# Performance work log

Measured on AMD Instinct MI355X. Metric: run time of the kernel, lower is better.

## Reference

```python
import jax, jax.numpy as jnp
import numpy as np

D = 256      # dim_model
H = 8        # n_head
FFN = 1024
L = 2        # n_layers
WIN = 100.0  # window_size of LocalisedEncoding
MINWL = 0.01 # min_wavelength of LocalisedEncoding
EPS = 1e-5


def _mass_sinusoid(mz):
    # depthcharge MassEncoder: min_wavelength=0.001, max_wavelength=10000
    n_sin = D // 2
    n_cos = D - n_sin
    base = 0.001 / (2.0 * np.pi)
    scale = 10000.0 / 0.001
    sin_term = (base * scale ** (np.arange(n_sin) / (n_sin - 1))).astype(np.float32)
    cos_term = (base * scale ** (np.arange(n_cos) / (n_cos - 1))).astype(np.float32)
    return jnp.concatenate([jnp.sin(mz / sin_term), jnp.cos(mz / cos_term)], axis=-1)


def _pe_lookup(pe, mass):
    # LocalisedEncoding.forward: clamp, linear index into precomputed table
    m = jnp.clip(mass, -WIN, WIN)
    idx = ((m + 1.0 + WIN) / MINWL).astype(jnp.int32)
    return pe[idx]


def _ln(x, g, b):
    mu = jnp.mean(x, axis=-1, keepdims=True)
    var = jnp.mean((x - mu) ** 2, axis=-1, keepdims=True)
    return (x - mu) * jax.lax.rsqrt(var + EPS) * g + b


def _forward(spectra, pe, latent, int_w, in_w, in_b, out_w, out_b,
             l1_w, l1_b, l2_w, l2_b, n1_g, n1_b, n2_g, n2_b):
    B, Np, _ = spectra.shape
    pad = jnp.sum(spectra, axis=2) == 0  # padded peaks
    # CustomPeakEncoder with mass=None, precursor_mass=None, dim_intensity=None
    peaks = _mass_sinusoid(spectra[:, :, :1]) + spectra[:, :, 1:2] @ int_w.T
    x = jnp.concatenate([jnp.broadcast_to(latent, (B, 1, D)), peaks], axis=1)
    mask = jnp.concatenate([jnp.zeros((B, 1), bool), pad], axis=1)  # [B,N]
    masses = jnp.concatenate([jnp.zeros((B, 1), spectra.dtype), spectra[:, :, 0]], axis=1)
    N = Np + 1
    hd = D // H
    scale = 1.0 / np.sqrt(hd)
    neg = jnp.asarray(-1e9, x.dtype)

    for l in range(L):
        wq, wk, wv = in_w[l, :D], in_w[l, D:2 * D], in_w[l, 2 * D:]
        bq, bk, bv = in_b[l, :D], in_b[l, D:2 * D], in_b[l, 2 * D:]
        if l == 0:
            # localized path: relative mass-difference encoding added to K/V
            pe0 = _pe_lookup(pe, jnp.zeros((), x.dtype))          # [D]
            q_in = x + pe0                                         # [B,N,D]
            rel = masses[:, None, :] - masses[:, :, None]          # m_j - m_i, [B,N,N]
            kv_in = x[:, None, :, :] + _pe_lookup(pe, rel)         # [B,N,N,D]
            Q = (q_in @ wq.T + bq).reshape(B, N, H, hd)
            K = (kv_in @ wk.T + bk).reshape(B, N, N, H, hd)
            V = (kv_in @ wv.T + bv).reshape(B, N, N, H, hd)
            s = jnp.einsum('bihd,bijhd->bhij', Q, K) * scale
            s = jnp.where(mask[:, None, None, :], neg, s)
            a = jax.nn.softmax(s, axis=-1)
            y = jnp.einsum('bhij,bijhd->bihd', a, V).reshape(B, N, D)
        else:
            Q = (x @ wq.T + bq).reshape(B, N, H, hd)
            K = (x @ wk.T + bk).reshape(B, N, H, hd)
            V = (x @ wv.T + bv).reshape(B, N, H, hd)
            s = jnp.einsum('bihd,bjhd->bhij', Q, K) * scale
            s = jnp.where(mask[:, None, None, :], neg, s)
            a = jax.nn.softmax(s, axis=-1)
            y = jnp.einsum('bhij,bjhd->bihd', a, V).reshape(B, N, D)
        y = y @ out_w[l].T + out_b[l]
        x = _ln(x + y, n1_g[l], n1_b[l])
        f = jax.nn.relu(x @ l1_w[l].T + l1_b[l]) @ l2_w[l].T + l2_b[l]
        x = _ln(x + f, n2_g[l], n2_b[l])
    return x


def setup_inputs() -> dict:
    key = jax.random.key(0)
    ks = jax.random.split(key, 14)
    B, Np = 16, 150
    mz = jax.random.uniform(ks[0], (B, Np, 1), dtype=jnp.float32) * 300.0
    inten = jax.random.uniform(ks[1], (B, Np, 1), dtype=jnp.float32)
    spectra = jnp.concatenate([mz, inten], axis=-1)
    # zero-pad the last 20 peaks of every other spectrum
    pad = (jnp.arange(Np)[None, :] >= 130) & (jnp.arange(B)[:, None] % 2 == 0)
    spectra = jnp.where(pad[:, :, None], 0.0, spectra)

    # LocalisedEncoding precomputed pe buffer (casanovo_style=True)
    max_len = int((WIN + 1) * 2 / MINWL)  # 20200
    pos = np.arange(max_len) - max_len // 2
    div = np.exp(np.arange(0, D, 2) * (-np.log(10000.0) / D))
    pe_np = np.zeros((max_len, D), np.float32)
    pe_np[:, : D // 2] = np.sin(pos[:, None] * div)
    pe_np[:, D // 2:] = np.cos(pos[:, None] * div)

    s = 0.05
    return {
        'spectra': spectra,
        'pe': jnp.asarray(pe_np),
        'latent': jax.random.normal(ks[2], (1, 1, D), jnp.float32) * s,
        'int_w': jax.random.normal(ks[3], (D, 1), jnp.float32) * s,
        'in_w': jax.random.normal(ks[4], (L, 3 * D, D), jnp.float32) * s,
        'in_b': jax.random.normal(ks[5], (L, 3 * D), jnp.float32) * s,
        'out_w': jax.random.normal(ks[6], (L, D, D), jnp.float32) * s,
        'out_b': jax.random.normal(ks[7], (L, D), jnp.float32) * s,
        'l1_w': jax.random.normal(ks[8], (L, FFN, D), jnp.float32) * s,
        'l1_b': jax.random.normal(ks[9], (L, FFN), jnp.float32) * s,
        'l2_w': jax.random.normal(ks[10], (L, D, FFN), jnp.float32) * s,
        'l2_b': jax.random.normal(ks[11], (L, D), jnp.float32) * s,
        'n1_g': jnp.ones((L, D), jnp.float32),
        'n1_b': jnp.zeros((L, D), jnp.float32),
        'n2_g': jnp.ones((L, D), jnp.float32),
        'n2_b': jnp.zeros((L, D), jnp.float32),
    }


def reference(spectra, pe, latent, int_w, in_w, in_b, out_w, out_b,
              l1_w, l1_b, l2_w, l2_b, n1_g, n1_b, n2_g, n2_b):
    return _forward(spectra, pe, latent, int_w, in_w, in_b, out_w, out_b,
                    l1_w, l1_b, l2_w, l2_b, n1_g, n1_b, n2_g, n2_b)
```

## Files before the change

kernel.cpp:

```cpp
#include <hip/hip_runtime.h>
#include <hip/hip_bf16.h>
#include <math.h>

#define BB 16
#define NP 150
#define NN 151
#define DD 256
#define HH 8
#define HD 32
#define FFN_ 1024
#define PE_LEN 20200
#define ROWS (BB*NN)
#define MPAD 2432
#define PE_PAD 20224


typedef __attribute__((ext_vector_type(8))) short short8;
typedef __attribute__((ext_vector_type(4))) float f32x4;
typedef __attribute__((ext_vector_type(4))) unsigned u32x4;

#if defined(__has_builtin)
#if __has_builtin(__builtin_amdgcn_fdot2_f32_bf16)
#define HAVE_DOT2 1
#endif
#endif
#ifndef HAVE_DOT2
#define HAVE_DOT2 0
#endif

__device__ __forceinline__ float r16(float x) {
    return __bfloat162float(__float2bfloat16(x));
}
__device__ __forceinline__ float us2f(unsigned short u) {
    return __uint_as_float((unsigned)u << 16);
}
__device__ __forceinline__ float lo2f(unsigned x) {
    return __uint_as_float(x << 16);
}
__device__ __forceinline__ float hi2f(unsigned x) {
    return __uint_as_float(x & 0xFFFF0000u);
}
__device__ __forceinline__ unsigned cvtpk(float lo, float hi) {
    unsigned r;
    asm("v_cvt_pk_bf16_f32 %0, %1, %2" : "=v"(r) : "v"(lo), "v"(hi));
    return r;
}
#if HAVE_DOT2
typedef __attribute__((ext_vector_type(2))) __bf16 bf16x2;
__device__ __forceinline__ float dot2bf(unsigned a, unsigned b, float acc) {
    bf16x2 av = __builtin_bit_cast(bf16x2, a);
    bf16x2 bv = __builtin_bit_cast(bf16x2, b);
    return __builtin_amdgcn_fdot2_f32_bf16(av, bv, acc, false);
}
#endif

#define PACK_BLOCKS 1024
__global__ __launch_bounds__(256) void buildpack_kernel(
    const float* __restrict__ spectra, const float* __restrict__ latent,
    const float* __restrict__ int_w, const float* __restrict__ pe,
    float* __restrict__ x, __hip_bfloat16* __restrict__ xb,
    __hip_bfloat16* __restrict__ xqb,
    float* __restrict__ masses, float* __restrict__ maskf,
    const float* __restrict__ in_w,  __hip_bfloat16* __restrict__ inw_p,
    const float* __restrict__ out_w, __hip_bfloat16* __restrict__ outw_p,
    const float* __restrict__ l1_w,  __hip_bfloat16* __restrict__ l1w_p,
    const float* __restrict__ l2_w,  __hip_bfloat16* __restrict__ l2w_p,
    __hip_bfloat16* __restrict__ pe_p)
{
    int tid = threadIdx.x;
    if (blockIdx.x < ROWS) {
        int bn = blockIdx.x;
        int b = bn / NN, n = bn % NN;
        float val;
        if (n == 0) {
            val = latent[tid];
            if (tid == 0) { masses[bn] = 0.0f; maskf[bn] = 0.0f; }
        } else {
            float mz = spectra[(b*NP + n - 1)*2 + 0];
            float it = spectra[(b*NP + n - 1)*2 + 1];
            int i = (tid < 128) ? tid : tid - 128;
            const double base_d = 0.001 / (2.0 * 3.141592653589793);
            double term_d = base_d * pow(1.0e7, (double)i / 127.0);
            float tf = (float)term_d;
            double arg = (double)mz / (double)tf;
            double sv = (tid < 128) ? sin(arg) : cos(arg);
            val = (float)sv + it * int_w[tid];
            if (tid == 0) {
                masses[bn] = mz;
                maskf[bn] = ((mz + it) == 0.0f) ? 1.0f : 0.0f;
            }
        }
        x[bn*DD + tid] = val;
        xb[bn*DD + tid] = __float2bfloat16(val);
        xqb[bn*DD + tid] = __float2bfloat16(val + pe[10100*DD + tid]);
    } else {
        long long base = (long long)(blockIdx.x - ROWS) * 256 + tid;
        const long long stride = (long long)PACK_BLOCKS * 256;
        for (long long i = base; i < (long long)PE_PAD*DD; i += stride)
            pe_p[i] = __float2bfloat16(i < (long long)PE_LEN*DD ? pe[i] : 0.0f);
        for (long long i = base; i < 2LL*768*DD; i += stride)
            inw_p[i] = __float2bfloat16(in_w[i]);
        for (long long i = base; i < 2LL*DD*DD; i += stride)
            outw_p[i] = __float2bfloat16(out_w[i]);
        for (long long i = base; i < 2LL*FFN_*DD; i += stride)
            l1w_p[i] = __float2bfloat16(l1_w[i]);
        for (long long i = base; i < 2LL*DD*FFN_; i += stride)
            l2w_p[i] = __float2bfloat16(l2_w[i]);
    }
}

template<typename CT>
__global__ __launch_bounds__(256) void gemm_mfma(
    const __hip_bfloat16* __restrict__ A, const __hip_bfloat16* __restrict__ W,
    const float* __restrict__ bias, CT* __restrict__ C,
    int M, int Nc, int K, int ldc, int relu)
{
    int wave = threadIdx.x >> 6;
    int lane = threadIdx.x & 63;
    int NT = Nc >> 5;
    int MT = (M + 31) >> 5;
    int id = blockIdx.x * 4 + wave;
    if (id >= MT * NT) return;
    int mt = id / NT, nt = id % NT;
    int m0 = mt * 32, n0 = nt * 32;
    int rl = lane & 15, q8 = (lane >> 4) * 8;

    const short8* Ap0 = (const short8*)(A + (size_t)(m0 + rl)*K + q8);
    const short8* Ap1 = (const short8*)(A + (size_t)(m0 + 16 + rl)*K + q8);
    const short8* Wp0 = (const short8*)(W + (size_t)(n0 + rl)*K + q8);
    const short8* Wp1 = (const short8*)(W + (size_t)(n0 + 16 + rl)*K + q8);

    f32x4 acc00 = {0,0,0,0}, acc01 = {0,0,0,0};
    f32x4 acc10 = {0,0,0,0}, acc11 = {0,0,0,0};
    int steps = K >> 5;
    for (int s = 0; s < steps; ++s) {
        short8 a0 = Ap0[s*4];
        short8 a1 = Ap1[s*4];
        short8 b0 = Wp0[s*4];
        short8 b1 = Wp1[s*4];
        acc00 = __builtin_amdgcn_mfma_f32_16x16x32_bf16(a0, b0, acc00, 0, 0, 0);
        acc01 = __builtin_amdgcn_mfma_f32_16x16x32_bf16(a0, b1, acc01, 0, 0, 0);
        acc10 = __builtin_amdgcn_mfma_f32_16x16x32_bf16(a1, b0, acc10, 0, 0, 0);
        acc11 = __builtin_amdgcn_mfma_f32_16x16x32_bf16(a1, b1, acc11, 0, 0, 0);
    }

    int rbase = (lane >> 4) * 4;
    #pragma unroll
    for (int sm = 0; sm < 2; ++sm) {
        #pragma unroll
        for (int sn = 0; sn < 2; ++sn) {
            f32x4 a = (sm == 0) ? (sn == 0 ? acc00 : acc01)
                                : (sn == 0 ? acc10 : acc11);
            int gc = n0 + sn*16 + rl;
            float bv = bias ? r16(bias[gc]) : 0.0f;
            #pragma unroll
            for (int rg = 0; rg < 4; ++rg) {
                int gr = m0 + sm*16 + rbase + rg;
                if (gr < M) {
                    float val = r16(a[rg]);
                    if (bias) val = r16(val + bv);
                    if (relu) val = fmaxf(val, 0.0f);
                    C[(size_t)gr*ldc + gc] = (CT)val;
                }
            }
        }
    }
}

template<int K>
__global__ __launch_bounds__(256) void gemm_skinny(
    const __hip_bfloat16* __restrict__ A, const __hip_bfloat16* __restrict__ W,
    const float* __restrict__ bias, float* __restrict__ C,
    int M, int Nc, int ldc)
{
    int NT = Nc >> 5;
    int id = blockIdx.x;
    int mt = id / NT, nt = id % NT;
    int m0 = mt * 16, n0 = nt * 32;
    int wave = threadIdx.x >> 6;
    int lane = threadIdx.x & 63;
    int rl = lane & 15, q8 = (lane >> 4) * 8;
    const int K4 = K >> 2;
    int k0 = wave * K4;

    const short8* Ap  = (const short8*)(A + (size_t)(m0 + rl)*K + k0 + q8);
    const short8* Wp0 = (const short8*)(W + (size_t)(n0 + rl)*K + k0 + q8);
    const short8* Wp1 = (const short8*)(W + (size_t)(n0 + 16 + rl)*K + k0 + q8);

    f32x4 acc0 = {0,0,0,0}, acc1 = {0,0,0,0};
    #pragma unroll
    for (int s = 0; s < K4/32; ++s) {
        short8 a  = Ap[s*4];
        short8 b0 = Wp0[s*4];
        short8 b1 = Wp1[s*4];
        acc0 = __builtin_amdgcn_mfma_f32_16x16x32_bf16(a, b0, acc0, 0, 0, 0);
        acc1 = __builtin_amdgcn_mfma_f32_16x16x32_bf16(a, b1, acc1, 0, 0, 0);
    }

    __shared__ float red[4][8][65];
    #pragma unroll
    for (int rg = 0; rg < 4; ++rg) {
        red[wave][rg][lane]   = acc0[rg];
        red[wave][4+rg][lane] = acc1[rg];
    }
    __syncthreads();

    #pragma unroll
    for (int t = 0; t < 2; ++t) {
        int sl = wave*2 + t;
        float s = red[0][sl][lane] + red[1][sl][lane]
                + red[2][sl][lane] + red[3][sl][lane];
        int rg = sl & 3, sn = sl >> 2;
        int gr = m0 + (lane >> 4)*4 + rg;
        int gc = n0 + sn*16 + rl;
        float val = r16(s);
        val = r16(val + r16(bias[gc]));
        if (gr < M) C[(size_t)gr*ldc + gc] = val;
    }
}

#define PEKV_BLK 632u
#define QKV0_BLK 456u

__device__ __forceinline__ void pekv_body(
    unsigned bid, int wave, int lane,
    const __hip_bfloat16* __restrict__ A, const __hip_bfloat16* __restrict__ W,
    __hip_bfloat16* __restrict__ C)
{
    const int K = 256, Nc = 512, ldc = 512, M = PE_LEN;
    int NT = Nc >> 5;
    int MT4 = (M + 127) >> 7;
    int id = bid * 4 + wave;
    if (id >= MT4 * NT) return;
    int mt = id / NT, nt = id % NT;
    int m0 = mt * 128, n0 = nt * 32;
    int rl = lane & 15, q8 = (lane >> 4) * 8;

    const short8* Ab  = (const short8*)(A + (size_t)(m0 + rl)*K + q8);
    const short8* Wp0 = (const short8*)(W + (size_t)(n0 + rl)*K + q8);
    const short8* Wp1 = (const short8*)(W + (size_t)(n0 + 16 + rl)*K + q8);
    const int rstep = K >> 3;

    f32x4 acc[4][2][2] = {};
    for (int s = 0; s < 8; ++s) {
        short8 b0 = Wp0[s*4];
        short8 b1 = Wp1[s*4];
        short8 a[4][2];
        #pragma unroll
        for (int t = 0; t < 4; ++t) {
            a[t][0] = Ab[(size_t)(t*32)*rstep + s*4];
            a[t][1] = Ab[(size_t)(t*32+16)*rstep + s*4];
        }
        #pragma unroll
        for (int t = 0; t < 4; ++t) {
            acc[t][0][0] = __builtin_amdgcn_mfma_f32_16x16x32_bf16(a[t][0], b0, acc[t][0][0], 0, 0, 0);
            acc[t][0][1] = __builtin_amdgcn_mfma_f32_16x16x32_bf16(a[t][0], b1, acc[t][0][1], 0, 0, 0);
            acc[t][1][0] = __builtin_amdgcn_mfma_f32_16x16x32_bf16(a[t][1], b0, acc[t][1][0], 0, 0, 0);
            acc[t][1][1] = __builtin_amdgcn_mfma_f32_16x16x32_bf16(a[t][1], b1, acc[t][1][1], 0, 0, 0);
        }
    }

    int rbase = (lane >> 4) * 4;
    #pragma unroll
    for (int t = 0; t < 4; ++t) {
        #pragma unroll
        for (int sm = 0; sm < 2; ++sm) {
            #pragma unroll
            for (int sn = 0; sn < 2; ++sn) {
                f32x4 a = acc[t][sm][sn];
                int gc = n0 + sn*16 + rl;
                #pragma unroll
                for (int rg = 0; rg < 4; ++rg) {
                    int gr = m0 + t*32 + sm*16 + rbase + rg;
                    if (gr < M)
                        C[(size_t)gr*ldc + gc] = (__hip_bfloat16)r16(a[rg]);
                }
            }
        }
    }
}

__device__ __forceinline__ void qkv0_body(
    unsigned bid, int wave, int lane,
    const __hip_bfloat16* __restrict__ xqb, const __hip_bfloat16* __restrict__ xb,
    const __hip_bfloat16* __restrict__ inw_p, const float* __restrict__ in_b,
    __hip_bfloat16* __restrict__ qb, __hip_bfloat16* __restrict__ kvb, int M)
{
    int MT = (M + 31) >> 5;
    int id = bid * 4 + wave;
    if (id >= MT * 24) return;
    int mt = id / 24, ntt = id % 24;
    bool isQ = (ntt < 8);
    const __hip_bfloat16* A = isQ ? xqb : xb;
    const __hip_bfloat16* W = inw_p + (isQ ? (size_t)ntt*32*DD
                                           : (size_t)(256 + (ntt-8)*32)*DD);
    const float* bias = in_b + (isQ ? ntt*32 : 256 + (ntt-8)*32);
    __hip_bfloat16* C = isQ ? qb : kvb;
    int ldc = isQ ? 256 : 512;
    int cbase = isQ ? ntt*32 : (ntt-8)*32;
    int m0 = mt * 32;
    int rl = lane & 15, q8 = (lane >> 4) * 8;
    const int K = DD;

    const short8* Ap0 = (const short8*)(A + (size_t)(m0 + rl)*K + q8);
    const short8* Ap1 = (const short8*)(A + (size_t)(m0 + 16 + rl)*K + q8);
    const short8* Wp0 = (const short8*)(W + (size_t)(rl)*K + q8);
    const short8* Wp1 = (const short8*)(W + (size_t)(16 + rl)*K + q8);

    f32x4 acc00 = {0,0,0,0}, acc01 = {0,0,0,0};
    f32x4 acc10 = {0,0,0,0}, acc11 = {0,0,0,0};
    for (int s = 0; s < K/32; ++s) {
        short8 a0 = Ap0[s*4];
        short8 a1 = Ap1[s*4];
        short8 b0 = Wp0[s*4];
        short8 b1 = Wp1[s*4];
        acc00 = __builtin_amdgcn_mfma_f32_16x16x32_bf16(a0, b0, acc00, 0, 0, 0);
        acc01 = __builtin_amdgcn_mfma_f32_16x16x32_bf16(a0, b1, acc01, 0, 0, 0);
        acc10 = __builtin_amdgcn_mfma_f32_16x16x32_bf16(a1, b0, acc10, 0, 0, 0);
        acc11 = __builtin_amdgcn_mfma_f32_16x16x32_bf16(a1, b1, acc11, 0, 0, 0);
    }

    int rbase = (lane >> 4) * 4;
    #pragma unroll
    for (int sm = 0; sm < 2; ++sm) {
        #pragma unroll
        for (int sn = 0; sn < 2; ++sn) {
            f32x4 a = (sm == 0) ? (sn == 0 ? acc00 : acc01)
                                : (sn == 0 ? acc10 : acc11);
            int gc = cbase + sn*16 + rl;
            float bv = r16(bias[sn*16 + rl]);
            #pragma unroll
            for (int rg = 0; rg < 4; ++rg) {
                int gr = m0 + sm*16 + rbase + rg;
                if (gr < M) {
                    float val = r16(a[rg]);
                    val = r16(val + bv);
                    C[(size_t)gr*ldc + gc] = (__hip_bfloat16)val;
                }
            }
        }
    }
}

__global__ __launch_bounds__(256) void pekv_qkv0_kernel(
    const __hip_bfloat16* __restrict__ pe_p, const __hip_bfloat16* __restrict__ wkv0,
    __hip_bfloat16* __restrict__ pekv,
    const __hip_bfloat16* __restrict__ xqb, const __hip_bfloat16* __restrict__ xb,
    const __hip_bfloat16* __restrict__ inw_p, const float* __restrict__ in_b,
    __hip_bfloat16* __restrict__ qb, __hip_bfloat16* __restrict__ kvb)
{
    int wave = threadIdx.x >> 6;
    int lane = threadIdx.x & 63;
    if (blockIdx.x < PEKV_BLK)
        pekv_body(blockIdx.x, wave, lane, pe_p, wkv0, pekv);
    else
        qkv0_body(blockIdx.x - PEKV_BLK, wave, lane, xqb, xb, inw_p, in_b,
                  qb, kvb, ROWS);
}

template<bool USE_PE, int QS, int KS, int VS>
__global__ __launch_bounds__(256) void attn_kernel(
    const __hip_bfloat16* __restrict__ qp,
    const __hip_bfloat16* __restrict__ kp,
    const __hip_bfloat16* __restrict__ vp,
    const __hip_bfloat16* __restrict__ pekv,
    const float* __restrict__ masses, const float* __restrict__ maskf,
    __hip_bfloat16* __restrict__ yb)
{
    int b = blockIdx.x & 15;
    int i = blockIdx.x >> 4;
    int tid = threadIdx.x;
    int c = tid & 31;
    int g = tid >> 5;
    int h = c >> 2;

    __shared__ float sc[HH][152];
    __shared__ float msh[152];
    __shared__ int   tj[152];
    __shared__ __align__(16) float part[8][264];

    if (tid < NN) {
        msh[tid] = maskf[b*NN + tid];
        if (USE_PE) {
            double m = (double)masses[b*NN + tid] - (double)masses[b*NN + i];
            m = fmin(fmax(m, -100.0), 100.0);
            tj[tid] = (int)(((m + 1.0) + 100.0) / 0.01);
        }
    }

    unsigned qw[4];
    {
        const u32x4 q4 = *(const u32x4*)((const unsigned short*)qp
                            + (size_t)(b*NN + i)*QS + c*8);
        qw[0] = q4[0]; qw[1] = q4[1]; qw[2] = q4[2]; qw[3] = q4[3];
    }
#if !HAVE_DOT2
    float qf[8];
    #pragma unroll
    for (int w = 0; w < 4; ++w) { qf[2*w] = lo2f(qw[w]); qf[2*w+1] = hi2f(qw[w]); }
#endif
    __syncthreads();

    const float scale = 0.17677669529663687f;
    const unsigned short* kbase = (const unsigned short*)kp + (size_t)(b*NN)*KS + c*8;
    const unsigned short* vbase = (const unsigned short*)vp + (size_t)(b*NN)*VS + c*8;
    const unsigned short* pkb = (const unsigned short*)pekv + c*8;
    const unsigned short* pvb = (const unsigned short*)pekv + 256 + c*8;

    {
        int j = g;
        u32x4 kcur = *(const u32x4*)(kbase + (size_t)j*KS);
        u32x4 pcur;
        if (USE_PE) pcur = *(const u32x4*)(pkb + (size_t)tj[j]*512);
        for (int p = 0; p < 19; ++p) {
            int jn = j + 8;
            bool more = (jn < NN);
            u32x4 kn, pn;
            if (more) {
                kn = *(const u32x4*)(kbase + (size_t)jn*KS);
                if (USE_PE) pn = *(const u32x4*)(pkb + (size_t)tj[jn]*512);
            }
            float acc = 0.0f;
#if HAVE_DOT2
            #pragma unroll
            for (int w = 0; w < 4; ++w) {
                unsigned kd = kcur[w];
                if (USE_PE) {
                    unsigned pd = pcur[w];
                    float s0 = lo2f(kd) + lo2f(pd);
                    float s1 = hi2f(kd) + hi2f(pd);
                    kd = cvtpk(s0, s1);
                }
                acc = dot2bf(qw[w], kd, acc);
            }
#else
            #pragma unroll
            for (int w = 0; w < 4; ++w) {
                unsigned kd = kcur[w];
                float k0 = lo2f(kd), k1 = hi2f(kd);
                if (USE_PE) {
                    unsigned pd = pcur[w];
                    k0 = r16(k0 + lo2f(pd));
                    k1 = r16(k1 + hi2f(pd));
                }
                acc = fmaf(qf[2*w], k0, acc);
                acc = fmaf(qf[2*w+1], k1, acc);
            }
#endif
            acc += __shfl_xor(acc, 1);
            acc += __shfl_xor(acc, 2);
            if ((c & 3) == 0) {
                float s = acc * scale;
                if (msh[j] != 0.0f) s = -1e9f;
                sc[h][j] = s;
            }
            if (!more) break;
            j = jn; kcur = kn;
            if (USE_PE) pcur = pn;
        }
    }
    __syncthreads();

    {
        int lane = tid & 31;
        int hh = g;
        float mx = -INFINITY;
        for (int j = lane; j < NN; j += 32) mx = fmaxf(mx, sc[hh][j]);
        #pragma unroll
        for (int off = 16; off; off >>= 1) mx = fmaxf(mx, __shfl_xor(mx, off, 32));
        float sum = 0.0f;
        for (int j = lane; j < NN; j += 32) {
            float e = expf(sc[hh][j] - mx);
            sc[hh][j] = e;
            sum += e;
        }
        #pragma unroll
        for (int off = 16; off; off >>= 1) sum += __shfl_xor(sum, off, 32);
        float inv = 1.0f / sum;
        for (int j = lane; j < NN; j += 32) sc[hh][j] = r16(sc[hh][j] * inv);
    }
    __syncthreads();

    {
        float ya[8];
        #pragma unroll
        for (int u = 0; u < 8; ++u) ya[u] = 0.0f;

#if HAVE_DOT2
        u32x4 vA = *(const u32x4*)(vbase + (size_t)g*VS);
        u32x4 vB = *(const u32x4*)(vbase + (size_t)(g+8)*VS);
        u32x4 pA, pB;
        if (USE_PE) {
            pA = *(const u32x4*)(pvb + (size_t)tj[g]*512);
            pB = *(const u32x4*)(pvb + (size_t)tj[g+8]*512);
        }
        for (int t = 0; t < 9; ++t) {
            int jA = g + t*16, jB = jA + 8;
            u32x4 nvA, nvB, npA, npB;
            if (t < 8) {
                int nA = jA + 16, nB = jB + 16;
                nvA = *(const u32x4*)(vbase + (size_t)nA*VS);
                nvB = *(const u32x4*)(vbase + (size_t)nB*VS);
                if (USE_PE) {
                    npA = *(const u32x4*)(pvb + (size_t)tj[nA]*512);
                    npB = *(const u32x4*)(pvb + (size_t)tj[nB]*512);
                }
            }
            unsigned apair = cvtpk(sc[h][jA], sc[h][jB]);
            #pragma unroll
            for (int w = 0; w < 4; ++w) {
                unsigned lopair, hipair;
                if (USE_PE) {
                    float sA0 = lo2f(vA[w]) + lo2f(pA[w]);
                    float sA1 = hi2f(vA[w]) + hi2f(pA[w]);
                    float sB0 = lo2f(vB[w]) + lo2f(pB[w]);
                    float sB1 = hi2f(vB[w]) + hi2f(pB[w]);
                    lopair = cvtpk(sA0, sB0);
                    hipair = cvtpk(sA1, sB1);
                } else {
                    lopair = __builtin_amdgcn_perm(vB[w], vA[w], 0x05040100u);
                    hipair = __builtin_amdgcn_perm(vB[w], vA[w], 0x07060302u);
                }
                ya[2*w]   = dot2bf(apair, lopair, ya[2*w]);
                ya[2*w+1] = dot2bf(apair, hipair, ya[2*w+1]);
            }
            if (t < 8) {
                vA = nvA; vB = nvB;
                if (USE_PE) { pA = npA; pB = npB; }
            }
        }
        if (g + 144 < NN) {
            int jT = g + 144;
            u32x4 v = *(const u32x4*)(vbase + (size_t)jT*VS);
            u32x4 pq;
            if (USE_PE) pq = *(const u32x4*)(pvb + (size_t)tj[jT]*512);
            float aT = sc[h][jT];
            #pragma unroll
            for (int w = 0; w < 4; ++w) {
                float v0 = lo2f(v[w]), v1 = hi2f(v[w]);
                if (USE_PE) {
                    unsigned pk2 = cvtpk(v0 + lo2f(pq[w]), v1 + hi2f(pq[w]));
                    v0 = lo2f(pk2); v1 = hi2f(pk2);
                }
                ya[2*w]   = fmaf(aT, v0, ya[2*w]);
                ya[2*w+1] = fmaf(aT, v1, ya[2*w+1]);
            }
        }
#else
        int j = g;
        u32x4 vcur = *(const u32x4*)(vbase + (size_t)j*VS);
        u32x4 pcur;
        if (USE_PE) pcur = *(const u32x4*)(pvb + (size_t)tj[j]*512);
        float acur = sc[h][j];
        for (int p = 0; p < 19; ++p) {
            int jn = j + 8;
            bool more = (jn < NN);
            u32x4 vn, pn;
            float an = 0.0f;
            if (more) {
                vn = *(const u32x4*)(vbase + (size_t)jn*VS);
                if (USE_PE) pn = *(const u32x4*)(pvb + (size_t)tj[jn]*512);
                an = sc[h][jn];
            }
            #pragma unroll
            for (int w = 0; w < 4; ++w) {
                float v0 = lo2f(vcur[w]), v1 = hi2f(vcur[w]);
                if (USE_PE) {
                    v0 = r16(v0 + lo2f(pcur[w]));
                    v1 = r16(v1 + hi2f(pcur[w]));
                }
                ya[2*w]   = fmaf(acur, v0, ya[2*w]);
                ya[2*w+1] = fmaf(acur, v1, ya[2*w+1]);
            }
            if (!more) break;
            j = jn; vcur = vn; acur = an;
            if (USE_PE) pcur = pn;
        }
#endif
        f32x4* pp = (f32x4*)&part[g][c*8];
        pp[0] = f32x4{ya[0], ya[1], ya[2], ya[3]};
        pp[1] = f32x4{ya[4], ya[5], ya[6], ya[7]};
    }
    __syncthreads();

    {
        float s = part[0][tid];
        #pragma unroll
        for (int g2 = 1; g2 < 8; ++g2) s += part[g2][tid];
        yb[(size_t)(b*NN + i)*DD + tid] = __float2bfloat16(s);
    }
}

template<bool WRITE_B>
__global__ __launch_bounds__(256) void add_ln_kernel(
    const float* __restrict__ xin, const float* __restrict__ res,
    const float* __restrict__ g, const float* __restrict__ bb,
    float* __restrict__ xout, __hip_bfloat16* __restrict__ xbout)
{
    int r = blockIdx.x; int tid = threadIdx.x;
    float v = xin[r*DD + tid] + res[r*DD + tid];
    __shared__ float red[4];
    float s = v;
    #pragma unroll
    for (int off = 32; off; off >>= 1) s += __shfl_xor(s, off);
    if ((tid & 63) == 0) red[tid >> 6] = s;
    __syncthreads();
    float mu = (red[0] + red[1] + red[2] + red[3]) * (1.0f/256.0f);
    __syncthreads();
    float d = v - mu;
    float s2 = d*d;
    #pragma unroll
    for (int off = 32; off; off >>= 1) s2 += __shfl_xor(s2, off);
    if ((tid & 63) == 0) red[tid >> 6] = s2;
    __syncthreads();
    float var = (red[0] + red[1] + red[2] + red[3]) * (1.0f/256.0f);
    float out = d * (1.0f / sqrtf(var + 1e-5f)) * g[tid] + bb[tid];
    xout[r*DD + tid] = out;
    if (WRITE_B) xbout[r*DD + tid] = __float2bfloat16(out);
}

extern "C" void kernel_launch(void* const* d_in, const int* in_sizes, int n_in,
                              void* d_out, int out_size, void* d_ws, size_t ws_size,
                              hipStream_t stream)
{
    const float* spectra = (const float*)d_in[0];
    const float* pe      = (const float*)d_in[1];
    const float* latent  = (const float*)d_in[2];
    const float* int_w   = (const float*)d_in[3];
    const float* in_w    = (const float*)d_in[4];
    const float* in_b    = (const float*)d_in[5];
    const float* out_w   = (const float*)d_in[6];
    const float* out_b   = (const float*)d_in[7];
    const float* l1_w    = (const float*)d_in[8];
    const float* l1_b    = (const float*)d_in[9];
    const float* l2_w    = (const float*)d_in[10];
    const float* l2_b    = (const float*)d_in[11];
    const float* n1_g    = (const float*)d_in[12];
    const float* n1_b    = (const float*)d_in[13];
    const float* n2_g    = (const float*)d_in[14];
    const float* n2_b    = (const float*)d_in[15];

    float* x      = (float*)d_ws;
    float* y2     = x      + ROWS*DD;
    float* masses = y2     + ROWS*DD;
    float* maskf  = masses + ROWS;
    __hip_bfloat16* bp = (__hip_bfloat16*)(maskf + ROWS);
    __hip_bfloat16* xb    = bp;  bp += (size_t)MPAD*DD;
    __hip_bfloat16* xqb   = bp;  bp += (size_t)MPAD*DD;
    __hip_bfloat16* qb    = bp;  bp += (size_t)MPAD*DD;
    __hip_bfloat16* kvb   = bp;  bp += (size_t)MPAD*768;
    __hip_bfloat16* yb    = bp;  bp += (size_t)MPAD*DD;
    __hip_bfloat16* f1b   = bp;  bp += (size_t)MPAD*FFN_;
    __hip_bfloat16* pekv  = bp;  bp += (size_t)PE_PAD*512;
    __hip_bfloat16* pe_p  = bp;  bp += (size_t)PE_PAD*DD;
    __hip_bfloat16* inw_p = bp;  bp += (size_t)2*768*DD;
    __hip_bfloat16* outw_p= bp;  bp += (size_t)2*DD*DD;
    __hip_bfloat16* l1w_p = bp;  bp += (size_t)2*FFN_*DD;
    __hip_bfloat16* l2w_p = bp;  bp += (size_t)2*DD*FFN_;

    dim3 blk(256);
    auto GG = [](int M, int Nc){ return dim3((unsigned)((((M+31)>>5)*(Nc>>5) + 3) / 4)); };
    const unsigned SKINNY = (ROWS/16) * (256 >> 5);

    buildpack_kernel<<<ROWS + PACK_BLOCKS, blk, 0, stream>>>(
        spectra, latent, int_w, pe, x, xb, xqb, masses, maskf,
        in_w, inw_p, out_w, outw_p, l1_w, l1w_p, l2_w, l2w_p, pe_p);

    pekv_qkv0_kernel<<<PEKV_BLK + QKV0_BLK, blk, 0, stream>>>(
        pe_p, inw_p + 256*DD, pekv, xqb, xb, inw_p, in_b, qb, kvb);

    attn_kernel<true,256,512,512><<<ROWS, blk, 0, stream>>>(
        qb, kvb, kvb + 256, pekv, masses, maskf, yb);
    gemm_skinny<256><<<SKINNY, blk, 0, stream>>>(
        yb, outw_p, out_b, y2, ROWS, 256, 256);
    add_ln_kernel<true><<<ROWS, blk, 0, stream>>>(x, y2, n1_g, n1_b, x, xb);
    gemm_mfma<__hip_bfloat16><<<GG(ROWS, 1024), blk, 0, stream>>>(
        xb, l1w_p, l1_b, f1b, ROWS, 1024, 256, 1024, 1);
    gemm_skinny<1024><<<SKINNY, blk, 0, stream>>>(
        f1b, l2w_p, l2_b, y2, ROWS, 256, 256);
    add_ln_kernel<true><<<ROWS, blk, 0, stream>>>(x, y2, n2_g, n2_b, x, xb);

    gemm_mfma<__hip_bfloat16><<<GG(ROWS, 768), blk, 0, stream>>>(
        xb, inw_p + 768*DD, in_b + 768, kvb, ROWS, 768, 256, 768, 0);
    attn_kernel<false,768,768,768><<<ROWS, blk, 0, stream>>>(
        kvb, kvb + 256, kvb + 512, nullptr, masses, maskf, yb);
    gemm_skinny<256><<<SKINNY, blk, 0, stream>>>(
        yb, outw_p + 256*DD, out_b + 256, y2, ROWS, 256, 256);
    add_ln_kernel<true><<<ROWS, blk, 0, stream>>>(x, y2, n1_g + 256, n1_b + 256, x, xb);
    gemm_mfma<__hip_bfloat16><<<GG(ROWS, 1024), blk, 0, stream>>>(
        xb, l1w_p + FFN_*DD, l1_b + 1024, f1b, ROWS, 1024, 256, 1024, 1);
    gemm_skinny<1024><<<SKINNY, blk, 0, stream>>>(
        f1b, l2w_p + DD*FFN_, l2_b + 256, y2, ROWS, 256, 256);
    add_ln_kernel<false><<<ROWS, blk, 0, stream>>>(x, y2, n2_g + 256, n2_b + 256,
                                                   (float*)d_out, nullptr);
}
```

Measured before the change: 304.0 us.

## Precompute Q·K attention scores with MFMA GEMM before attention kernels

Adds a gemm_sqk kernel that computes the per-head Q·K^T score matrices with 16x16x32 bf16 MFMA into a padded fp32 workspace. The attention kernels then load these scores instead of doing scalar dot products against K. In layer 0 only the Q·PE_k term is still computed in-kernel and added to the loaded score. This replaces scalar score work with matrix instructions, but adds two kernel launches and an fp32 score buffer round trip through global memory. It also changes rounding, since (q·k + q·pe) is no longer the dot product of q with the bf16-rounded k+pe.

```diff
diff --git a/kernel.cpp b/kernel.cpp
--- a/kernel.cpp
+++ b/kernel.cpp
@@ -13,6 +13,7 @@
 #define ROWS (BB*NN)
 #define MPAD 2432
 #define PE_PAD 20224
+#define SQS 160
 
 
 typedef __attribute__((ext_vector_type(8))) short short8;
@@ -219,6 +220,35 @@
     }
 }
 
+template<int QS, int KS>
+__global__ __launch_bounds__(256) void gemm_sqk(
+    const __hip_bfloat16* __restrict__ Q, const __hip_bfloat16* __restrict__ Kp,
+    float* __restrict__ S)
+{
+    int wave = threadIdx.x >> 6;
+    int lane = threadIdx.x & 63;
+    int id = blockIdx.x * 4 + wave;
+    if (id >= 16*8*100) return;
+    int jt = id % 10, it = (id / 10) % 10;
+    int h = (id / 100) & 7, b = id / 800;
+    int i0 = it * 16, j0 = jt * 16;
+    int rl = lane & 15, q8 = (lane >> 4) * 8;
+
+    short8 a  = *(const short8*)(Q  + (size_t)(b*NN + i0 + rl)*QS + h*32 + q8);
+    short8 kb = *(const short8*)(Kp + (size_t)(b*NN + j0 + rl)*KS + h*32 + q8);
+    f32x4 acc = {0,0,0,0};
+    acc = __builtin_amdgcn_mfma_f32_16x16x32_bf16(a, kb, acc, 0, 0, 0);
+
+    float* Sb = S + ((size_t)(b*8 + h))*SQS*SQS;
+    int rbase = (lane >> 4) * 4;
+    #pragma unroll
+    for (int rg = 0; rg < 4; ++rg) {
+        int ii = i0 + rbase + rg, jj = j0 + rl;
+        if (ii < NN && jj < NN)
+            Sb[(size_t)ii*SQS + jj] = acc[rg];
+    }
+}
+
 #define PEKV_BLK 632u
 #define QKV0_BLK 456u
 
@@ -358,12 +388,12 @@
                   qb, kvb, ROWS);
 }
 
-template<bool USE_PE, int QS, int KS, int VS>
+template<bool USE_PE, int QS, int VS>
 __global__ __launch_bounds__(256) void attn_kernel(
     const __hip_bfloat16* __restrict__ qp,
-    const __hip_bfloat16* __restrict__ kp,
     const __hip_bfloat16* __restrict__ vp,
     const __hip_bfloat16* __restrict__ pekv,
+    const float* __restrict__ sqk,
     const float* __restrict__ masses, const float* __restrict__ maskf,
     __hip_bfloat16* __restrict__ yb)
 {
@@ -373,6 +403,7 @@
     int c = tid & 31;
     int g = tid >> 5;
     int h = c >> 2;
+    const float scale = 0.17677669529663687f;
 
     __shared__ float sc[HH][152];
     __shared__ float msh[152];
@@ -380,86 +411,77 @@
     __shared__ __align__(16) float part[8][264];
 
     if (tid < NN) {
-        msh[tid] = maskf[b*NN + tid];
+        float mval = maskf[b*NN + tid];
+        msh[tid] = mval;
         if (USE_PE) {
             double m = (double)masses[b*NN + tid] - (double)masses[b*NN + i];
             m = fmin(fmax(m, -100.0), 100.0);
             tj[tid] = (int)(((m + 1.0) + 100.0) / 0.01);
         }
+        const float* Sb = sqk + ((size_t)(b*8))*SQS*SQS + (size_t)i*SQS + tid;
+        if (USE_PE) {
+            #pragma unroll
+            for (int hh = 0; hh < 8; ++hh)
+                sc[hh][tid] = Sb[(size_t)hh*SQS*SQS];
+        } else {
+            #pragma unroll
+            for (int hh = 0; hh < 8; ++hh) {
+                float s = Sb[(size_t)hh*SQS*SQS] * scale;
+                sc[hh][tid] = (mval != 0.0f) ? -1e9f : s;
+            }
+        }
     }
 
     unsigned qw[4];
-    {
+#if !HAVE_DOT2
+    float qf[8];
+#endif
+    if (USE_PE) {
         const u32x4 q4 = *(const u32x4*)((const unsigned short*)qp
                             + (size_t)(b*NN + i)*QS + c*8);
         qw[0] = q4[0]; qw[1] = q4[1]; qw[2] = q4[2]; qw[3] = q4[3];
-    }
 #if !HAVE_DOT2
-    float qf[8];
-    #pragma unroll
-    for (int w = 0; w < 4; ++w) { qf[2*w] = lo2f(qw[w]); qf[2*w+1] = hi2f(qw[w]); }
+        #pragma unroll
+        for (int w = 0; w < 4; ++w) { qf[2*w] = lo2f(qw[w]); qf[2*w+1] = hi2f(qw[w]); }
 #endif
+    }
     __syncthreads();
 
-    const float scale = 0.17677669529663687f;
-    const unsigned short* kbase = (const unsigned short*)kp + (size_t)(b*NN)*KS + c*8;
     const unsigned short* vbase = (const unsigned short*)vp + (size_t)(b*NN)*VS + c*8;
     const unsigned short* pkb = (const unsigned short*)pekv + c*8;
     const unsigned short* pvb = (const unsigned short*)pekv + 256 + c*8;
 
-    {
+    if (USE_PE) {
         int j = g;
-        u32x4 kcur = *(const u32x4*)(kbase + (size_t)j*KS);
-        u32x4 pcur;
-        if (USE_PE) pcur = *(const u32x4*)(pkb + (size_t)tj[j]*512);
+        u32x4 pcur = *(const u32x4*)(pkb + (size_t)tj[j]*512);
         for (int p = 0; p < 19; ++p) {
             int jn = j + 8;
             bool more = (jn < NN);
-            u32x4 kn, pn;
-            if (more) {
-                kn = *(const u32x4*)(kbase + (size_t)jn*KS);
-                if (USE_PE) pn = *(const u32x4*)(pkb + (size_t)tj[jn]*512);
-            }
+            u32x4 pn;
+            if (more) pn = *(const u32x4*)(pkb + (size_t)tj[jn]*512);
             float acc = 0.0f;
 #if HAVE_DOT2
             #pragma unroll
+            for (int w = 0; w < 4; ++w) acc = dot2bf(qw[w], pcur[w], acc);
+#else
+            #pragma unroll
             for (int w = 0; w < 4; ++w) {
-                unsigned kd = kcur[w];
-                if (USE_PE) {
-                    unsigned pd = pcur[w];
-                    float s0 = lo2f(kd) + lo2f(pd);
-                    float s1 = hi2f(kd) + hi2f(pd);
-                    kd = cvtpk(s0, s1);
-                }
-                acc = dot2bf(qw[w], kd, acc);
-            }
-#else
-            #pragma unroll
-            for (int w = 0; w < 4; ++w) {
-                unsigned kd = kcur[w];
-                float k0 = lo2f(kd), k1 = hi2f(kd);
-                if (USE_PE) {
-                    unsigned pd = pcur[w];
-                    k0 = r16(k0 + lo2f(pd));
-                    k1 = r16(k1 + hi2f(pd));
-                }
-                acc = fmaf(qf[2*w], k0, acc);
-                acc = fmaf(qf[2*w+1], k1, acc);
+                acc = fmaf(qf[2*w],   lo2f(pcur[w]), acc);
+                acc = fmaf(qf[2*w+1], hi2f(pcur[w]), acc);
             }
 #endif
             acc += __shfl_xor(acc, 1);
             acc += __shfl_xor(acc, 2);
             if ((c & 3) == 0) {
-                float s = acc * scale;
+                float s = (sc[h][j] + acc) * scale;
                 if (msh[j] != 0.0f) s = -1e9f;
                 sc[h][j] = s;
             }
             if (!more) break;
-            j = jn; kcur = kn;
-            if (USE_PE) pcur = pn;
-        }
-    }
-    __syncthreads();
+            j = jn; pcur = pn;
+        }
+        __syncthreads();
+    }
 
     {
         int lane = tid & 31;
@@ -644,7 +666,8 @@
     float* y2     = x      + ROWS*DD;
     float* masses = y2     + ROWS*DD;
     float* maskf  = masses + ROWS;
-    __hip_bfloat16* bp = (__hip_bfloat16*)(maskf + ROWS);
+    float* sqkb   = maskf  + ROWS;
+    __hip_bfloat16* bp = (__hip_bfloat16*)(sqkb + (size_t)16*8*SQS*SQS);
     __hip_bfloat16* xb    = bp;  bp += (size_t)MPAD*DD;
     __hip_bfloat16* xqb   = bp;  bp += (size_t)MPAD*DD;
     __hip_bfloat16* qb    = bp;  bp += (size_t)MPAD*DD;
@@ -660,7 +683,8 @@
 
     dim3 blk(256);
     auto GG = [](int M, int Nc){ return dim3((unsigned)((((M+31)>>5)*(Nc>>5) + 3) / 4)); };
-    const unsigned SKINNY = (ROWS/16) * (256 >> 5);
+    const unsigned SK256 = (ROWS/16) * (256 >> 5);
+    const unsigned SQKG  = (16*8*100 + 3) / 4;
 
     buildpack_kernel<<<ROWS + PACK_BLOCKS, blk, 0, stream>>>(
         spectra, latent, int_w, pe, x, xb, xqb, masses, maskf,
@@ -669,27 +693,29 @@
     pekv_qkv0_kernel<<<PEKV_BLK + QKV0_BLK, blk, 0, stream>>>(
         pe_p, inw_p + 256*DD, pekv, xqb, xb, inw_p, in_b, qb, kvb);
 
-    attn_kernel<true,256,512,512><<<ROWS, blk, 0, stream>>>(
-        qb, kvb, kvb + 256, pekv, masses, maskf, yb);
-    gemm_skinny<256><<<SKINNY, blk, 0, stream>>>(
+    gemm_sqk<256,512><<<SQKG, blk, 0, stream>>>(qb, kvb, sqkb);
+    attn_kernel<true,256,512><<<ROWS, blk, 0, stream>>>(
+        qb, kvb + 256, pekv, sqkb, masses, maskf, yb);
+    gemm_skinny<256><<<SK256, blk, 0, stream>>>(
         yb, outw_p, out_b, y2, ROWS, 256, 256);
     add_ln_kernel<true><<<ROWS, blk, 0, stream>>>(x, y2, n1_g, n1_b, x, xb);
     gemm_mfma<__hip_bfloat16><<<GG(ROWS, 1024), blk, 0, stream>>>(
         xb, l1w_p, l1_b, f1b, ROWS, 1024, 256, 1024, 1);
-    gemm_skinny<1024><<<SKINNY, blk, 0, stream>>>(
+    gemm_skinny<1024><<<SK256, blk, 0, stream>>>(
         f1b, l2w_p, l2_b, y2, ROWS, 256, 256);
     add_ln_kernel<true><<<ROWS, blk, 0, stream>>>(x, y2, n2_g, n2_b, x, xb);
 
     gemm_mfma<__hip_bfloat16><<<GG(ROWS, 768), blk, 0, stream>>>(
         xb, inw_p + 768*DD, in_b + 768, kvb, ROWS, 768, 256, 768, 0);
-    attn_kernel<false,768,768,768><<<ROWS, blk, 0, stream>>>(
-        kvb, kvb + 256, kvb + 512, nullptr, masses, maskf, yb);
-    gemm_skinny<256><<<SKINNY, blk, 0, stream>>>(
+    gemm_sqk<768,768><<<SQKG, blk, 0, stream>>>(kvb, kvb + 256, sqkb);
+    attn_kernel<false,768,768><<<ROWS, blk, 0, stream>>>(
+        kvb, kvb + 512, nullptr, sqkb, masses, maskf, yb);
+    gemm_skinny<256><<<SK256, blk, 0, stream>>>(
         yb, outw_p + 256*DD, out_b + 256, y2, ROWS, 256, 256);
     add_ln_kernel<true><<<ROWS, blk, 0, stream>>>(x, y2, n1_g + 256, n1_b + 256, x, xb);
     gemm_mfma<__hip_bfloat16><<<GG(ROWS, 1024), blk, 0, stream>>>(
         xb, l1w_p + FFN_*DD, l1_b + 1024, f1b, ROWS, 1024, 256, 1024, 1);
-    gemm_skinny<1024><<<SKINNY, blk, 0, stream>>>(
+    gemm_skinny<1024><<<SK256, blk, 0, stream>>>(
         f1b, l2w_p + DD*FFN_, l2_b + 256, y2, ROWS, 256, 256);
     add_ln_kernel<false><<<ROWS, blk, 0, stream>>>(x, y2, n2_g + 256, n2_b + 256,
                                                    (float*)d_out, nullptr);
```

Result: no change. 302.8 us (-0.4%).
